# Kernel optimization log

Measured on AMD Instinct MI355X. Metric: run time of the kernel, lower is better.

Reference implementation:

```python
import jax, jax.numpy as jnp
import numpy as np

CH, XH, YH, RADIUS = 2, 2, 2, 1  # channel_heads, x_heads, y_heads, neighborhood radius


def neighborhood_mask(n_sub_x, n_sub_y, radius):
    # clamped neighbor offsets reduce to |di|<=r and |dj|<=r within the grid
    iy = jnp.arange(n_sub_y)
    ix = jnp.arange(n_sub_x)
    my = jnp.abs(iy[:, None] - iy[None, :]) <= radius  # [ny, ny]
    mx = jnp.abs(ix[:, None] - ix[None, :]) <= radius  # [nx, nx]
    m = my[:, None, :, None] & mx[None, :, None, :]    # [ny, nx, ny, nx]
    s = n_sub_x * n_sub_y
    return m.reshape(s, s)  # row-major (h1 w1)(h2 w2), matching einops


def setup_inputs() -> dict:
    key = jax.random.key(0)
    k1, k2, k3 = jax.random.split(key, 3)
    C = 128
    seq = jax.random.normal(k1, (2, 256, C, 16, 16), dtype=jnp.float32)
    w_qkv = jax.random.normal(k2, (3 * C, C), dtype=jnp.float32) / np.sqrt(C).astype(np.float32)
    w_out = jax.random.normal(k3, (C, C), dtype=jnp.float32) / np.sqrt(C).astype(np.float32)
    b_out = jnp.zeros((C,), dtype=jnp.float32)
    return {"seq": seq, "w_qkv": w_qkv, "w_out": w_out, "b_out": b_out,
            "n_sub_x": 16, "n_sub_y": 16}


def reference(seq, w_qkv, w_out, b_out, n_sub_x, n_sub_y):
    b, s, C, H, W = seq.shape
    h, w = H // YH, W // XH
    c = C // CH
    nH = YH * XH * CH  # total heads

    # pointwise qkv projection over channels: [b, s, 3C, H, W]
    qkv = jnp.einsum('bschw,dc->bsdhw', seq, w_qkv)

    # decompose2d: split spatial grid into y_heads x x_heads blocks -> spatial heads
    # [b, s, 3C, YH, h, XH, w] -> [b, s, YH*XH, 3C, h, w]
    qkv = qkv.reshape(b, s, 3 * C, YH, h, XH, w)
    qkv = qkv.transpose(0, 1, 3, 5, 2, 4, 6).reshape(b, s, YH * XH, 3 * C, h, w)

    # split into q,k,v and channel heads: 3C = 3 * CH * c
    qkv = qkv.reshape(b, s, YH * XH, 3, CH, c, h, w)
    # -> [3, b, (spatial_heads * channel_heads), s, c, h, w]
    qkv = qkv.transpose(3, 0, 2, 4, 1, 5, 6, 7).reshape(3, b, nH, s, c, h, w)
    q, k, v = qkv[0], qkv[1], qkv[2]

    # scaled dot-product attention over flattened function dim (c,h,w)
    scale = 1.0 / np.sqrt(c * h * w).astype(np.float32)
    scores = jnp.einsum('bnschw,bntchw->bnst', q, k) * scale  # [b, nH, s, s]
    mask = neighborhood_mask(n_sub_x, n_sub_y, RADIUS)  # [s, s]
    scores = jnp.where(mask[None, None, :, :], scores, jnp.finfo(scores.dtype).min)
    attn = jax.nn.softmax(scores, axis=-1)
    sa = jnp.einsum('bnst,bntchw->bnschw', attn, v)  # [b, nH, s, c, h, w]

    # merge channel heads back: [b, s, spatial_heads, C, h, w]
    sa = sa.reshape(b, YH * XH, CH, s, c, h, w)
    sa = sa.transpose(0, 3, 1, 2, 4, 5, 6).reshape(b, s, YH, XH, C, h, w)
    # recompose2d: [b, s, C, H, W]
    sa = sa.transpose(0, 1, 4, 2, 5, 3, 6).reshape(b, s, C, H, W)

    # output pointwise projection with bias
    out = jnp.einsum('bschw,dc->bsdhw', sa, w_out) + b_out[None, None, :, None, None]
    return out
```

## Files before the change

### kernel.cpp

```cpp
#include <hip/hip_runtime.h>

#define BATCH 2
#define SS    256
#define CC    128
#define HWN   256
#define FDIM  4096

typedef unsigned int uint;
typedef unsigned short ushort;
typedef short bf16x8 __attribute__((ext_vector_type(8)));
typedef ushort us4 __attribute__((ext_vector_type(4)));
typedef float f32x4 __attribute__((ext_vector_type(4)));

__device__ __forceinline__ ushort f2b(float f) {
  uint u = __float_as_uint(f);
  return (ushort)((u + 0x7fffu + ((u >> 16) & 1u)) >> 16);
}
__device__ __forceinline__ float b2f(ushort h) { return __uint_as_float((uint)h << 16); }

__global__ __launch_bounds__(512, 4) void k_qkv(const float* __restrict__ seq,
                                                const float* __restrict__ wqkv,
                                                ushort* __restrict__ qkvh) {
  __shared__ ushort wlds[128 * 128];
  const int bs = blockIdx.x;
  const int b = bs >> 8, s = bs & 255;
  const int t = threadIdx.x;
  const int wv = t >> 6, lane = t & 63;
  const int qq = lane >> 4, m = lane & 15;

  const float* sp = seq + (size_t)bs * (CC * HWN);

  bf16x8 bfrag[2][4];
  uint obase[2];
  #pragma unroll
  for (int set = 0; set < 2; ++set) {
    const int ntg = wv * 2 + set;
    const int hw = ntg * 16 + m;
    #pragma unroll
    for (int ks = 0; ks < 4; ++ks) {
      const int k0 = ks * 32 + qq * 8;
      float tmp[8];
      #pragma unroll
      for (int j = 0; j < 8; ++j) tmp[j] = sp[(k0 + j) * HWN + hw];
      bf16x8 fr;
      #pragma unroll
      for (int j = 0; j < 8; ++j) fr[j] = (short)f2b(tmp[j]);
      bfrag[set][ks] = fr;
    }
    const int n_qk = ((ntg >> 3) * 2 + (m >> 3)) * 2;
    const int hwl  = (ntg & 7) * 8 + (m & 7);
    obase[set] = (uint)(((b * 8 + n_qk) * SS + s) * FDIM + hwl * 16 + qq * 4);
  }

  for (int qkvi = 0; qkvi < 3; ++qkvi) {
    if (qkvi) __syncthreads();
    #pragma unroll
    for (int i = 0; i < 4; ++i) {
      const int row = i * 32 + (t >> 4), col16 = t & 15;
      const float* wp = wqkv + (size_t)(qkvi * 128 + row) * 128 + col16 * 8;
      f32x4 w0 = *(const f32x4*)(wp);
      f32x4 w1 = *(const f32x4*)(wp + 4);
      bf16x8 fr;
      #pragma unroll
      for (int e = 0; e < 4; ++e) { fr[e] = (short)f2b(w0[e]); fr[4 + e] = (short)f2b(w1[e]); }
      *(bf16x8*)&wlds[row * 128 + ((col16 ^ (row & 15)) * 8)] = fr;
    }
    __syncthreads();

    #pragma unroll
    for (int mt8 = 0; mt8 < 8; ++mt8) {
      bf16x8 afrag[4];
      #pragma unroll
      for (int ks = 0; ks < 4; ++ks)
        afrag[ks] = *(const bf16x8*)&wlds[(mt8 * 16 + m) * 128 + (((ks * 4 + qq) ^ m) * 8)];
      const int ch = mt8 >> 2, m4 = mt8 & 3;
      #pragma unroll
      for (int set = 0; set < 2; ++set) {
        f32x4 acc = {0.f, 0.f, 0.f, 0.f};
        #pragma unroll
        for (int ks = 0; ks < 4; ++ks)
          acc = __builtin_amdgcn_mfma_f32_16x16x32_bf16(afrag[ks], bfrag[set][ks], acc, 0, 0, 0);
        us4 pk;
        #pragma unroll
        for (int r = 0; r < 4; ++r) pk[r] = f2b(acc[r]);
        *(us4*)(qkvh + obase[set]
                + (uint)((qkvi * 16 + ch) * (SS * FDIM) + m4 * 1024)) = pk;
      }
    }
  }
}

__global__ __launch_bounds__(1024) void k_scores(const ushort* __restrict__ qkvh,
                                                 float* __restrict__ attn) {
  __shared__ float red[16][64][12];
  const int g = blockIdx.x;
  const int unit = (g & 7) * 32 + (g >> 3);
  const int b  = unit >> 7;
  const int n  = (unit >> 4) & 7;
  const int sy = unit & 15;
  const int t = threadIdx.x;
  const int wave = t >> 6, lane = t & 63;
  const int qq = lane >> 4, l15 = lane & 15;
  const size_t hs = (size_t)SS * FDIM;
  const ushort* qb = qkvh + (size_t)(b * 8 + n) * hs;
  const ushort* kb = qkvh + (size_t)(16 + b * 8 + n) * hs;

  const ushort* qp = qb + (size_t)(sy * 16 + l15) * FDIM + qq * 8;
  const ushort* kp[3];
  #pragma unroll
  for (int tl = 0; tl < 3; ++tl) {
    const int tyc = min(max(sy - 1 + tl, 0), 15);
    kp[tl] = kb + (size_t)(tyc * 16 + l15) * FDIM + qq * 8;
  }

  f32x4 acc[3] = {{0,0,0,0},{0,0,0,0},{0,0,0,0}};
  const int kbeg = wave * 256;
  #pragma unroll
  for (int it = 0; it < 4; ++it) {
    const int k0 = kbeg + it * 64;
    bf16x8 a0 = *(const bf16x8*)(qp + k0);
    bf16x8 a1 = *(const bf16x8*)(qp + k0 + 32);
    bf16x8 b0[3], b1[3];
    #pragma unroll
    for (int tl = 0; tl < 3; ++tl) {
      b0[tl] = *(const bf16x8*)(kp[tl] + k0);
      b1[tl] = *(const bf16x8*)(kp[tl] + k0 + 32);
    }
    #pragma unroll
    for (int tl = 0; tl < 3; ++tl)
      acc[tl] = __builtin_amdgcn_mfma_f32_16x16x32_bf16(a0, b0[tl], acc[tl], 0, 0, 0);
    #pragma unroll
    for (int tl = 0; tl < 3; ++tl)
      acc[tl] = __builtin_amdgcn_mfma_f32_16x16x32_bf16(a1, b1[tl], acc[tl], 0, 0, 0);
  }

  #pragma unroll
  for (int tl = 0; tl < 3; ++tl)
    #pragma unroll
    for (int r = 0; r < 4; ++r) red[wave][lane][tl * 4 + r] = acc[tl][r];
  __syncthreads();
  if (t < 768) {
    const int lane2 = t / 12, idx = t - lane2 * 12;
    float ssum = red[0][lane2][idx];
    #pragma unroll
    for (int w = 1; w < 16; ++w) ssum += red[w][lane2][idx];
    red[0][lane2][idx] = ssum;
  }
  __syncthreads();
  if (wave != 0) return;
  #pragma unroll
  for (int tl = 0; tl < 3; ++tl)
    #pragma unroll
    for (int r = 0; r < 4; ++r) acc[tl][r] = red[0][lane][tl * 4 + r];

  const int tx = l15;
  float sc[3][4];
  #pragma unroll
  for (int tl = 0; tl < 3; ++tl) {
    const int ty = sy - 1 + tl;
    const bool tyv = (ty >= 0 && ty < 16);
    #pragma unroll
    for (int r = 0; r < 4; ++r) {
      const int sx = qq * 4 + r;
      const bool v = tyv && (tx - sx <= 1) && (sx - tx <= 1);
      sc[tl][r] = v ? acc[tl][r] * (1.f / 64.f) : -1e30f;
    }
  }
  #pragma unroll
  for (int r = 0; r < 4; ++r) {
    float mx = fmaxf(fmaxf(sc[0][r], sc[1][r]), sc[2][r]);
    #pragma unroll
    for (int off = 1; off < 16; off <<= 1) mx = fmaxf(mx, __shfl_xor(mx, off));
    float p[3], sum = 0.f;
    #pragma unroll
    for (int tl = 0; tl < 3; ++tl) { p[tl] = __expf(sc[tl][r] - mx); sum += p[tl]; }
    #pragma unroll
    for (int off = 1; off < 16; off <<= 1) sum += __shfl_xor(sum, off);
    const float inv = 1.f / sum;
    const int sx = qq * 4 + r;
    const int s = sy * 16 + sx;
    #pragma unroll
    for (int tl = 0; tl < 3; ++tl) {
      const int ty = sy - 1 + tl;
      const int dxp = tx - sx + 1;
      if (ty >= 0 && ty < 16 && dxp >= 0 && dxp <= 2)
        attn[((size_t)(b * 8 + n) * SS + s) * 9 + tl * 3 + dxp] = p[tl] * inv;
    }
  }
}

__global__ __launch_bounds__(256) void k_pv(const ushort* __restrict__ qkvh,
                                            const float* __restrict__ attn,
                                            ushort* __restrict__ sa) {
  const int g = blockIdx.x;
  const int unit = (g & 7) * 512 + (g >> 3);
  const int eta = unit >> 8, s = unit & 255;
  const int sy = s >> 4, sx = s & 15;
  const int t = threadIdx.x;
  const size_t hs = (size_t)SS * FDIM;

  float p[9];
  int sjc[9];
  bool vld[9];
  #pragma unroll
  for (int j = 0; j < 9; ++j) {
    const int ny = sy + j / 3 - 1, nx = sx + j % 3 - 1;
    vld[j] = (ny >= 0 && ny < 16 && nx >= 0 && nx < 16);
    sjc[j] = min(max(ny, 0), 15) * 16 + min(max(nx, 0), 15);
    p[j] = vld[j] ? attn[((size_t)eta * SS + s) * 9 + j] : 0.f;
  }

  const ushort* vb = qkvh + (size_t)(32 + eta) * hs;
  const int f0 = t * 16;
  float acc[16];
  #pragma unroll
  for (int e = 0; e < 16; ++e) acc[e] = 0.f;
  #pragma unroll
  for (int j = 0; j < 9; ++j) {
    if (vld[j]) {
      const ushort* vp = vb + (size_t)sjc[j] * FDIM + f0;
      bf16x8 v0 = *(const bf16x8*)(vp);
      bf16x8 v1 = *(const bf16x8*)(vp + 8);
      const float pj = p[j];
      #pragma unroll
      for (int e = 0; e < 8; ++e) acc[e]     += pj * b2f((ushort)v0[e]);
      #pragma unroll
      for (int e = 0; e < 8; ++e) acc[8 + e] += pj * b2f((ushort)v1[e]);
    }
  }
  bf16x8 r0, r1;
  #pragma unroll
  for (int e = 0; e < 8; ++e) { r0[e] = (short)f2b(acc[e]); r1[e] = (short)f2b(acc[8 + e]); }
  ushort* op = sa + ((size_t)eta * SS + s) * FDIM + f0;
  *(bf16x8*)op = r0;
  *(bf16x8*)(op + 8) = r1;
}

__global__ __launch_bounds__(256) void k_proj(const ushort* __restrict__ qkvh,
                                              const float* __restrict__ wout,
                                              const float* __restrict__ bout,
                                              float* __restrict__ out) {
  __shared__ ushort wlds[128 * 128];
  const int g = blockIdx.x;
  const int r9 = g >> 3;
  const int G = (g & 7) * 4 + (r9 >> 6);
  const int idx = r9 & 63;
  const int b = G >> 4, sy = G & 15;
  const int sx = idx >> 2, sub = idx & 3;
  const int s = sy * 16 + sx;
  const int bs = b * 256 + s;
  const int t = threadIdx.x;
  const int wave = t >> 6, lane = t & 63;
  const int ntg = sub * 4 + wave;
  const int qq = lane >> 4, m = lane & 15;
  const size_t hs = (size_t)SS * FDIM;

  {
    const int col16 = t & 15;
    const int ks = col16 >> 2, qw = col16 & 3;
    const int creal0 = (ks >> 1) * 64 + ((((ks & 1) << 1) | (qw >> 1)) << 4)
                       + ((qw & 1) << 3);
    #pragma unroll
    for (int i = 0; i < 8; ++i) {
      const int row = i * 16 + (t >> 4);
      const float* wp = wout + (size_t)row * 128 + creal0;
      f32x4 w0 = *(const f32x4*)(wp);
      f32x4 w1 = *(const f32x4*)(wp + 4);
      bf16x8 fr;
      #pragma unroll
      for (int e = 0; e < 4; ++e) { fr[e] = (short)f2b(w0[e]); fr[4 + e] = (short)f2b(w1[e]); }
      *(bf16x8*)&wlds[row * 128 + ((col16 ^ (row & 15)) * 8)] = fr;
    }
  }

  const int nbase = ((ntg >> 3) * 2 + (m >> 3)) * 2;
  const int hwl = (ntg & 7) * 8 + (m & 7);
  bf16x8 bfrag[4];
  #pragma unroll
  for (int ks = 0; ks < 4; ++ks) {
    const int ch = ks >> 1;
    const int c64hi = ((ks & 1) << 1) | (qq >> 1);
    const int half = qq & 1;
    const ushort* sb = qkvh + (size_t)(b * 8 + nbase + ch) * hs;
    const int off = c64hi * 1024 + hwl * 16 + half * 8;
    bfrag[ks] = *(const bf16x8*)(sb + (size_t)s * FDIM + off);
  }

  __syncthreads();

  #pragma unroll
  for (int mt = 0; mt < 8; ++mt) {
    bf16x8 afrag[4];
    #pragma unroll
    for (int ks = 0; ks < 4; ++ks)
      afrag[ks] = *(const bf16x8*)&wlds[(mt * 16 + m) * 128 + (((ks * 4 + qq) ^ m) * 8)];
    f32x4 acc = {0.f, 0.f, 0.f, 0.f};
    #pragma unroll
    for (int ks = 0; ks < 4; ++ks)
      acc = __builtin_amdgcn_mfma_f32_16x16x32_bf16(afrag[ks], bfrag[ks], acc, 0, 0, 0);
    const int hw = ntg * 16 + m;
    #pragma unroll
    for (int r = 0; r < 4; ++r) {
      const int d = mt * 16 + qq * 4 + r;
      out[((size_t)bs * CC + d) * HWN + hw] = acc[r] + bout[d];
    }
  }
}

extern "C" void kernel_launch(void* const* d_in, const int* in_sizes, int n_in,
                              void* d_out, int out_size, void* d_ws, size_t ws_size,
                              hipStream_t stream) {
  const float* seq  = (const float*)d_in[0];
  const float* wqkv = (const float*)d_in[1];
  const float* wout = (const float*)d_in[2];
  const float* bout = (const float*)d_in[3];
  char* ws = (char*)d_ws;
  ushort* qkvh = (ushort*)(ws);
  float*  attn = (float*)(ws + 100663296ull);
  float*  outp = (float*)d_out;

  hipLaunchKernelGGL(k_qkv,    dim3(512),  dim3(512),  0, stream, seq, wqkv, qkvh);
  hipLaunchKernelGGL(k_scores, dim3(256),  dim3(1024), 0, stream, qkvh, attn);
  hipLaunchKernelGGL(k_pv,     dim3(4096), dim3(256),  0, stream, qkvh, attn, qkvh );
  hipLaunchKernelGGL(k_proj,   dim3(2048), dim3(256),  0, stream, qkvh, wout, bout, outp);
}
```

Before: 195.2 us.

## Restructure QKV staging via LDS, split score reduction with atomics, add softmax kernel

k_qkv now keeps the weight fragments in registers and stages the bf16-converted input tile in swizzled LDS with coalesced vector loads, replacing the per-qkvi weight LDS refills. k_scores is split across 4x more blocks, and partial dot products are accumulated into attn with atomicAdd instead of an in-block LDS reduction. A separate k_softmax kernel normalizes afterwards, and k_qkv zeroes attn beforehand. k_pv switches to nontemporal stores. The goal is better occupancy and coalescing, at the cost of an extra launch, atomics, and ordering that depends on k_qkv zeroing attn.

```diff
diff --git a/kernel.cpp b/kernel.cpp
--- a/kernel.cpp
+++ b/kernel.cpp
@@ -20,90 +20,91 @@
 
 __global__ __launch_bounds__(512, 4) void k_qkv(const float* __restrict__ seq,
                                                 const float* __restrict__ wqkv,
-                                                ushort* __restrict__ qkvh) {
-  __shared__ ushort wlds[128 * 128];
+                                                ushort* __restrict__ qkvh,
+                                                float* __restrict__ attn) {
+  __shared__ ushort sq[256 * 128];
   const int bs = blockIdx.x;
   const int b = bs >> 8, s = bs & 255;
   const int t = threadIdx.x;
   const int wv = t >> 6, lane = t & 63;
   const int qq = lane >> 4, m = lane & 15;
 
-  const float* sp = seq + (size_t)bs * (CC * HWN);
-
-  bf16x8 bfrag[2][4];
-  uint obase[2];
-  #pragma unroll
-  for (int set = 0; set < 2; ++set) {
-    const int ntg = wv * 2 + set;
-    const int hw = ntg * 16 + m;
+  if (blockIdx.x < 36) {
+    attn[blockIdx.x * 1024 + t] = 0.f;
+    attn[blockIdx.x * 1024 + 512 + t] = 0.f;
+  }
+
+  bf16x8 afrag[3][4];
+  #pragma unroll
+  for (int qkvi = 0; qkvi < 3; ++qkvi)
     #pragma unroll
     for (int ks = 0; ks < 4; ++ks) {
-      const int k0 = ks * 32 + qq * 8;
-      float tmp[8];
-      #pragma unroll
-      for (int j = 0; j < 8; ++j) tmp[j] = sp[(k0 + j) * HWN + hw];
-      bf16x8 fr;
-      #pragma unroll
-      for (int j = 0; j < 8; ++j) fr[j] = (short)f2b(tmp[j]);
-      bfrag[set][ks] = fr;
-    }
-    const int n_qk = ((ntg >> 3) * 2 + (m >> 3)) * 2;
-    const int hwl  = (ntg & 7) * 8 + (m & 7);
-    obase[set] = (uint)(((b * 8 + n_qk) * SS + s) * FDIM + hwl * 16 + qq * 4);
-  }
-
-  for (int qkvi = 0; qkvi < 3; ++qkvi) {
-    if (qkvi) __syncthreads();
-    #pragma unroll
-    for (int i = 0; i < 4; ++i) {
-      const int row = i * 32 + (t >> 4), col16 = t & 15;
-      const float* wp = wqkv + (size_t)(qkvi * 128 + row) * 128 + col16 * 8;
+      const float* wp = wqkv + (size_t)(qkvi * 128 + wv * 16 + m) * 128 + ks * 32 + qq * 8;
       f32x4 w0 = *(const f32x4*)(wp);
       f32x4 w1 = *(const f32x4*)(wp + 4);
       bf16x8 fr;
       #pragma unroll
       for (int e = 0; e < 4; ++e) { fr[e] = (short)f2b(w0[e]); fr[4 + e] = (short)f2b(w1[e]); }
-      *(bf16x8*)&wlds[row * 128 + ((col16 ^ (row & 15)) * 8)] = fr;
-    }
-    __syncthreads();
-
-    #pragma unroll
-    for (int mt8 = 0; mt8 < 8; ++mt8) {
-      bf16x8 afrag[4];
+      afrag[qkvi][ks] = fr;
+    }
+
+  const float* sp = seq + (size_t)bs * (CC * HWN);
+  #pragma unroll
+  for (int i = 0; i < 8; ++i) {
+    const int c2 = i * 8 + wv;
+    const int hw0 = lane * 4;
+    f32x4 va = *(const f32x4*)(sp + (size_t)(2 * c2) * HWN + hw0);
+    f32x4 vb = *(const f32x4*)(sp + (size_t)(2 * c2 + 1) * HWN + hw0);
+    #pragma unroll
+    for (int j = 0; j < 4; ++j) {
+      const int hw = hw0 + j;
+      const uint w = (uint)f2b(va[j]) | ((uint)f2b(vb[j]) << 16);
+      const int slot = (c2 >> 2) ^ (hw & 15) ^ ((hw >> 4) & 15);
+      *(uint*)((char*)sq + hw * 256 + slot * 16 + (c2 & 3) * 4) = w;
+    }
+  }
+  __syncthreads();
+
+  const int ch = wv >> 2, m4 = wv & 3;
+  #pragma unroll 2
+  for (int ntg = 0; ntg < 16; ++ntg) {
+    const int hw = ntg * 16 + m;
+    bf16x8 bfr[4];
+    #pragma unroll
+    for (int ks = 0; ks < 4; ++ks) {
+      const int slot = (ks * 4 + qq) ^ m ^ ntg;
+      bfr[ks] = *(const bf16x8*)((const char*)sq + hw * 256 + slot * 16);
+    }
+    const int n_qk = ((ntg >> 3) * 2 + (m >> 3)) * 2;
+    const int hwl  = (ntg & 7) * 8 + (m & 7);
+    const uint obase = (uint)(((b * 8 + n_qk) * SS + s) * FDIM + hwl * 16 + qq * 4);
+    #pragma unroll
+    for (int qkvi = 0; qkvi < 3; ++qkvi) {
+      f32x4 acc = {0.f, 0.f, 0.f, 0.f};
       #pragma unroll
       for (int ks = 0; ks < 4; ++ks)
-        afrag[ks] = *(const bf16x8*)&wlds[(mt8 * 16 + m) * 128 + (((ks * 4 + qq) ^ m) * 8)];
-      const int ch = mt8 >> 2, m4 = mt8 & 3;
-      #pragma unroll
-      for (int set = 0; set < 2; ++set) {
-        f32x4 acc = {0.f, 0.f, 0.f, 0.f};
-        #pragma unroll
-        for (int ks = 0; ks < 4; ++ks)
-          acc = __builtin_amdgcn_mfma_f32_16x16x32_bf16(afrag[ks], bfrag[set][ks], acc, 0, 0, 0);
-        us4 pk;
-        #pragma unroll
-        for (int r = 0; r < 4; ++r) pk[r] = f2b(acc[r]);
-        *(us4*)(qkvh + obase[set]
-                + (uint)((qkvi * 16 + ch) * (SS * FDIM) + m4 * 1024)) = pk;
-      }
-    }
-  }
-}
-
-__global__ __launch_bounds__(1024) void k_scores(const ushort* __restrict__ qkvh,
-                                                 float* __restrict__ attn) {
-  __shared__ float red[16][64][12];
+        acc = __builtin_amdgcn_mfma_f32_16x16x32_bf16(afrag[qkvi][ks], bfr[ks], acc, 0, 0, 0);
+      us4 pk;
+      #pragma unroll
+      for (int r = 0; r < 4; ++r) pk[r] = f2b(acc[r]);
+      *(us4*)(qkvh + obase + (uint)((qkvi * 16 + ch) * (SS * FDIM) + m4 * 1024)) = pk;
+    }
+  }
+}
+
+__global__ __launch_bounds__(256) void k_scores(const ushort* __restrict__ qkvh,
+                                                float* __restrict__ attn) {
   const int g = blockIdx.x;
-  const int unit = (g & 7) * 32 + (g >> 3);
-  const int b  = unit >> 7;
-  const int n  = (unit >> 4) & 7;
-  const int sy = unit & 15;
+  const int unit = (g & 7) * 128 + (g >> 3);
+  const int cg = unit & 3;
+  const int sy = (unit >> 2) & 15;
+  const int bn = unit >> 6;
   const int t = threadIdx.x;
   const int wave = t >> 6, lane = t & 63;
   const int qq = lane >> 4, l15 = lane & 15;
   const size_t hs = (size_t)SS * FDIM;
-  const ushort* qb = qkvh + (size_t)(b * 8 + n) * hs;
-  const ushort* kb = qkvh + (size_t)(16 + b * 8 + n) * hs;
+  const ushort* qb = qkvh + (size_t)bn * hs;
+  const ushort* kb = qkvh + (size_t)(16 + bn) * hs;
 
   const ushort* qp = qb + (size_t)(sy * 16 + l15) * FDIM + qq * 8;
   const ushort* kp[3];
@@ -114,7 +115,7 @@
   }
 
   f32x4 acc[3] = {{0,0,0,0},{0,0,0,0},{0,0,0,0}};
-  const int kbeg = wave * 256;
+  const int kbeg = (cg * 4 + wave) * 256;
   #pragma unroll
   for (int it = 0; it < 4; ++it) {
     const int k0 = kbeg + it * 64;
@@ -134,59 +135,49 @@
       acc[tl] = __builtin_amdgcn_mfma_f32_16x16x32_bf16(a1, b1[tl], acc[tl], 0, 0, 0);
   }
 
-  #pragma unroll
-  for (int tl = 0; tl < 3; ++tl)
-    #pragma unroll
-    for (int r = 0; r < 4; ++r) red[wave][lane][tl * 4 + r] = acc[tl][r];
-  __syncthreads();
-  if (t < 768) {
-    const int lane2 = t / 12, idx = t - lane2 * 12;
-    float ssum = red[0][lane2][idx];
-    #pragma unroll
-    for (int w = 1; w < 16; ++w) ssum += red[w][lane2][idx];
-    red[0][lane2][idx] = ssum;
-  }
-  __syncthreads();
-  if (wave != 0) return;
-  #pragma unroll
-  for (int tl = 0; tl < 3; ++tl)
-    #pragma unroll
-    for (int r = 0; r < 4; ++r) acc[tl][r] = red[0][lane][tl * 4 + r];
-
   const int tx = l15;
-  float sc[3][4];
   #pragma unroll
   for (int tl = 0; tl < 3; ++tl) {
     const int ty = sy - 1 + tl;
-    const bool tyv = (ty >= 0 && ty < 16);
+    if (ty < 0 || ty > 15) continue;
     #pragma unroll
     for (int r = 0; r < 4; ++r) {
       const int sx = qq * 4 + r;
-      const bool v = tyv && (tx - sx <= 1) && (sx - tx <= 1);
-      sc[tl][r] = v ? acc[tl][r] * (1.f / 64.f) : -1e30f;
-    }
-  }
-  #pragma unroll
-  for (int r = 0; r < 4; ++r) {
-    float mx = fmaxf(fmaxf(sc[0][r], sc[1][r]), sc[2][r]);
-    #pragma unroll
-    for (int off = 1; off < 16; off <<= 1) mx = fmaxf(mx, __shfl_xor(mx, off));
-    float p[3], sum = 0.f;
-    #pragma unroll
-    for (int tl = 0; tl < 3; ++tl) { p[tl] = __expf(sc[tl][r] - mx); sum += p[tl]; }
-    #pragma unroll
-    for (int off = 1; off < 16; off <<= 1) sum += __shfl_xor(sum, off);
-    const float inv = 1.f / sum;
-    const int sx = qq * 4 + r;
-    const int s = sy * 16 + sx;
-    #pragma unroll
-    for (int tl = 0; tl < 3; ++tl) {
-      const int ty = sy - 1 + tl;
-      const int dxp = tx - sx + 1;
-      if (ty >= 0 && ty < 16 && dxp >= 0 && dxp <= 2)
-        attn[((size_t)(b * 8 + n) * SS + s) * 9 + tl * 3 + dxp] = p[tl] * inv;
-    }
-  }
+      const int dx = tx - sx + 1;
+      if (dx >= 0 && dx <= 2)
+        atomicAdd(&attn[((size_t)bn * SS + sy * 16 + sx) * 9 + tl * 3 + dx], acc[tl][r]);
+    }
+  }
+}
+
+__global__ __launch_bounds__(256) void k_softmax(float* __restrict__ attn) {
+  const int id = blockIdx.x * 256 + threadIdx.x;
+  const int s = id & 255, sy = s >> 4, sx = s & 15;
+  float* ap = attn + (size_t)id * 9;
+  float v[9];
+  bool vld[9];
+  #pragma unroll
+  for (int j = 0; j < 9; ++j) {
+    v[j] = ap[j];
+    const int ny = sy + j / 3 - 1, nx = sx + j % 3 - 1;
+    vld[j] = (ny >= 0 && ny < 16 && nx >= 0 && nx < 16);
+  }
+  float mx = -1e30f;
+  float sc[9];
+  #pragma unroll
+  for (int j = 0; j < 9; ++j) {
+    sc[j] = vld[j] ? v[j] * (1.f / 64.f) : -1e30f;
+    mx = fmaxf(mx, sc[j]);
+  }
+  float p[9], sum = 0.f;
+  #pragma unroll
+  for (int j = 0; j < 9; ++j) {
+    p[j] = vld[j] ? __expf(sc[j] - mx) : 0.f;
+    sum += p[j];
+  }
+  const float inv = 1.f / sum;
+  #pragma unroll
+  for (int j = 0; j < 9; ++j) ap[j] = p[j] * inv;
 }
 
 __global__ __launch_bounds__(256) void k_pv(const ushort* __restrict__ qkvh,
@@ -232,8 +223,8 @@
   #pragma unroll
   for (int e = 0; e < 8; ++e) { r0[e] = (short)f2b(acc[e]); r1[e] = (short)f2b(acc[8 + e]); }
   ushort* op = sa + ((size_t)eta * SS + s) * FDIM + f0;
-  *(bf16x8*)op = r0;
-  *(bf16x8*)(op + 8) = r1;
+  __builtin_nontemporal_store(r0, (bf16x8*)op);
+  __builtin_nontemporal_store(r1, (bf16x8*)(op + 8));
 }
 
 __global__ __launch_bounds__(256) void k_proj(const ushort* __restrict__ qkvh,
@@ -319,8 +310,9 @@
   float*  attn = (float*)(ws + 100663296ull);
   float*  outp = (float*)d_out;
 
-  hipLaunchKernelGGL(k_qkv,    dim3(512),  dim3(512),  0, stream, seq, wqkv, qkvh);
-  hipLaunchKernelGGL(k_scores, dim3(256),  dim3(1024), 0, stream, qkvh, attn);
-  hipLaunchKernelGGL(k_pv,     dim3(4096), dim3(256),  0, stream, qkvh, attn, qkvh );
-  hipLaunchKernelGGL(k_proj,   dim3(2048), dim3(256),  0, stream, qkvh, wout, bout, outp);
-}
+  hipLaunchKernelGGL(k_qkv,     dim3(512),  dim3(512), 0, stream, seq, wqkv, qkvh, attn);
+  hipLaunchKernelGGL(k_scores,  dim3(1024), dim3(256), 0, stream, qkvh, attn);
+  hipLaunchKernelGGL(k_softmax, dim3(16),   dim3(256), 0, stream, attn);
+  hipLaunchKernelGGL(k_pv,      dim3(4096), dim3(256), 0, stream, qkvh, attn, qkvh );
+  hipLaunchKernelGGL(k_proj,    dim3(2048), dim3(256), 0, stream, qkvh, wout, bout, outp);
+}
```

Result: slower. 229.1 us (+17.3%).
